# Performance work log

Measured on AMD Instinct MI355X. Metric: run time of the kernel, lower is better.

Reference implementation:

```python
import jax, jax.numpy as jnp
import numpy as np
from jax import lax

# Building physics constants from metadata defaults (sqft=2000)
C_VAL = 300000.0 * 2000.0          # 6e8 J/K
R_VAL = 1.0 / (0.001 * 2000.0)     # 0.5 K/W
T_SET = (70.0 - 32.0) * 5.0 / 9.0  # ~21.111 C (mean of 68F/72F setpoints)
DELTA_T = 2.0
DT = 3600.0
T0 = 22.0
LAM_RC, LAM_COMFORT, LAM_SMOOTH = 1.0, 0.1, 0.01


def setup_inputs() -> dict:
    key = jax.random.key(0)
    k1, k2, k3 = jax.random.split(key, 3)
    B, T = 2048, 8760
    y_hat = jax.random.normal(k1, (B, T), dtype=jnp.float32)
    y_true = jax.random.normal(k2, (B, T), dtype=jnp.float32)
    T_out = jax.random.normal(k3, (B, T), dtype=jnp.float32)
    return {"y_hat": y_hat, "y_true": y_true, "T_out": T_out}


def _infer_temperature(y_hat, T_out):
    # Linear recurrence: T[t+1] = T[t] + dt/C * ((T_out[t]-T[t])/R + 1000*y_hat[t]/C)
    yW = y_hat * 1000.0
    T0v = jnp.full((y_hat.shape[0],), T0, dtype=y_hat.dtype)

    def step(Tc, inp):
        to_t, yw_t = inp
        Tn = Tc + (DT / C_VAL) * ((to_t - Tc) / R_VAL + yw_t / C_VAL)
        return Tn, Tn

    # scan over time; inputs are (T-1, B)
    _, Ts = lax.scan(step, T0v, (T_out[:, :-1].T, yW[:, :-1].T))
    return jnp.concatenate([T0v[:, None], Ts.T], axis=1)  # (B, T)


def reference(y_hat, y_true, T_out):
    # Data-fitting loss (MSE)
    l_data = jnp.mean((y_hat - y_true) ** 2)

    # Infer indoor temperature from RC dynamics
    T_hat = _infer_temperature(y_hat, T_out)

    # RC energy-balance residual loss
    dT = (T_hat[:, 1:] - T_hat[:, :-1]) / DT
    rhs = (T_out[:, :-1] - T_hat[:, :-1]) / R_VAL + (y_hat[:, :-1] * 1000.0) / C_VAL
    l_rc = jnp.mean((dT - rhs) ** 2)

    # Comfort-zone violation loss
    l_comfort = jnp.mean(jax.nn.relu(jnp.abs(T_hat - T_SET) - DELTA_T))

    # Second-order smoothness loss
    d2y = y_hat[:, 2:] - 2.0 * y_hat[:, 1:-1] + y_hat[:, :-2]
    l_smooth = jnp.mean(d2y ** 2)

    return l_data + LAM_RC * l_rc + LAM_COMFORT * l_comfort + LAM_SMOOTH * l_smooth
```

## Files before the change

kernel.cpp:

```cpp
#include <hip/hip_runtime.h>
#include <math.h>

namespace {

constexpr int B_ROWS = 2048;
constexpr int T_LEN  = 8760;
constexpr int NSTEP  = T_LEN - 1;
constexpr int BT     = 256;
constexpr int SEG    = 8;
constexpr int TILE   = BT * SEG;
constexpr int NTILE  = (T_LEN + TILE - 1) / TILE;

constexpr double dpow(double b, int e) { double r = 1.0; for (int i = 0; i < e; ++i) r *= b; return r; }

constexpr double A_D   = 1.0 - 1.2e-5;
constexpr float  AF    = (float)A_D;
constexpr float  A8F   = (float)dpow(A_D, SEG);
constexpr float  QWAVE = (float)dpow(A_D, SEG * 64);

constexpr float DTC    = 6.0e-6f;
constexpr float INV_R  = 2.0f;
constexpr float YC     = (float)(1000.0 / 6.0e8);
constexpr float INV_DT = (float)(1.0 / 3600.0);
constexpr float TSET   = (float)((70.0 - 32.0) * 5.0 / 9.0);
constexpr float TINIT  = 22.0f;

constexpr float W_DATA = (float)(1.0  / ((double)B_ROWS * T_LEN));
constexpr float W_RC   = (float)(1.0  / ((double)B_ROWS * (T_LEN - 1)));
constexpr float W_COMF = (float)(0.1  / ((double)B_ROWS * T_LEN));
constexpr float W_SM   = (float)(0.01 / ((double)B_ROWS * (T_LEN - 2)));

}

__global__ __launch_bounds__(BT) void pinn_main(const float* __restrict__ yh,
                                                const float* __restrict__ ytrue,
                                                const float* __restrict__ tout,
                                                float* __restrict__ ws) {
  const int tid  = threadIdx.x;
  const int lane = tid & 63;
  const int wv   = tid >> 6;
  const size_t rowoff = (size_t)blockIdx.x * T_LEN;
  const float* __restrict__ yr = yh    + rowoff;
  const float* __restrict__ ur = ytrue + rowoff;
  const float* __restrict__ tr = tout  + rowoff;

  float Alane = 1.0f;
  {
    float p = A8F; int e = lane;
    #pragma unroll
    for (int it = 0; it < 6; ++it) { if (e & 1) Alane *= p; p *= p; e >>= 1; }
  }

  __shared__ float sWave[4];
  __shared__ float sRed[4];

  float accData = 0.f, accRc = 0.f, accComf = 0.f, accSm = 0.f;
  float Ttile = TINIT;

  for (int tile = 0; tile < NTILE; ++tile) {
    const int segStart = tile * TILE + tid * SEG;
    const bool inb = segStart < T_LEN;
    float yv[SEG], tv[SEG];

    if (inb) {
      const float4 a0 = *reinterpret_cast<const float4*>(yr + segStart);
      const float4 a1 = *reinterpret_cast<const float4*>(yr + segStart + 4);
      const float4 b0 = *reinterpret_cast<const float4*>(tr + segStart);
      const float4 b1 = *reinterpret_cast<const float4*>(tr + segStart + 4);
      const float4 c0 = *reinterpret_cast<const float4*>(ur + segStart);
      const float4 c1 = *reinterpret_cast<const float4*>(ur + segStart + 4);
      yv[0]=a0.x; yv[1]=a0.y; yv[2]=a0.z; yv[3]=a0.w;
      yv[4]=a1.x; yv[5]=a1.y; yv[6]=a1.z; yv[7]=a1.w;
      tv[0]=b0.x; tv[1]=b0.y; tv[2]=b0.z; tv[3]=b0.w;
      tv[4]=b1.x; tv[5]=b1.y; tv[6]=b1.z; tv[7]=b1.w;
      float uv[SEG];
      uv[0]=c0.x; uv[1]=c0.y; uv[2]=c0.z; uv[3]=c0.w;
      uv[4]=c1.x; uv[5]=c1.y; uv[6]=c1.z; uv[7]=c1.w;
      #pragma unroll
      for (int i = 0; i < SEG; ++i) { const float d = yv[i] - uv[i]; accData += d * d; }
    } else {
      #pragma unroll
      for (int i = 0; i < SEG; ++i) { yv[i] = 0.f; tv[i] = 0.f; }
    }

    float yn0 = 0.f, yn1 = 0.f;
    if (inb && (segStart + SEG) < T_LEN) {
      yn0 = yr[segStart + SEG];
      yn1 = yr[segStart + SEG + 1];
    }

    if (inb) {
      #pragma unroll
      for (int i = 0; i < SEG; ++i) {
        const int t = segStart + i;
        if (t < T_LEN - 2) {
          const float y1 = (i < SEG - 1) ? yv[i + 1] : yn0;
          const float y2 = (i < SEG - 2) ? yv[i + 2] : ((i == SEG - 2) ? yn0 : yn1);
          const float d2 = y2 - 2.f * y1 + yv[i];
          accSm += d2 * d2;
        }
      }
    }

    float S = 0.f;
    #pragma unroll
    for (int i = 0; i < SEG; ++i) {
      const float f = DTC * (tv[i] * INV_R + yv[i] * YC);
      S = AF * S + f;
    }

    float inc = S;
    float m = A8F;
    #pragma unroll
    for (int d = 1; d < 64; d <<= 1) {
      const float up = __shfl_up(inc, (unsigned)d, 64);
      if (lane >= d) inc += m * up;
      m *= m;
    }
    float Eex = __shfl_up(inc, 1u, 64);
    if (lane == 0) Eex = 0.f;

    if (lane == 63) sWave[wv] = inc;
    __syncthreads();

    float W = Ttile;
    for (int v = 0; v < wv; ++v) W = QWAVE * W + sWave[v];
    float Tnext = Ttile;
    #pragma unroll
    for (int v = 0; v < 4; ++v) Tnext = QWAVE * Tnext + sWave[v];
    __syncthreads();
    Ttile = Tnext;

    float Tc = Alane * W + Eex;
    if (inb) {
      #pragma unroll
      for (int i = 0; i < SEG; ++i) {
        const int t = segStart + i;
        if (t < NSTEP) {
          const float rhs = (tv[i] - Tc) * INV_R + yv[i] * YC;
          const float Tnv = Tc + DTC * rhs;
          const float r = (Tnv - Tc) * INV_DT - rhs;
          accRc += r * r;
          const float c = fabsf(Tc - TSET) - 2.0f;
          accComf += (c > 0.f) ? c : 0.f;
          if (t == NSTEP - 1) {
            const float c2 = fabsf(Tnv - TSET) - 2.0f;
            accComf += (c2 > 0.f) ? c2 : 0.f;
          }
          Tc = Tnv;
        }
      }
    }
  }

  float total = accData * W_DATA + accRc * W_RC + accComf * W_COMF + accSm * W_SM;
  #pragma unroll
  for (int d = 32; d > 0; d >>= 1) total += __shfl_down(total, (unsigned)d, 64);
  if (lane == 0) sRed[wv] = total;
  __syncthreads();
  if (tid == 0) ws[blockIdx.x] = sRed[0] + sRed[1] + sRed[2] + sRed[3];
}

__global__ __launch_bounds__(256) void pinn_reduce(const float* __restrict__ ws,
                                                   float* __restrict__ out) {
  const int tid = threadIdx.x;
  float s = 0.f;
  for (int i = tid; i < B_ROWS; i += 256) s += ws[i];
  #pragma unroll
  for (int d = 32; d > 0; d >>= 1) s += __shfl_down(s, (unsigned)d, 64);
  __shared__ float sr[4];
  if ((tid & 63) == 0) sr[tid >> 6] = s;
  __syncthreads();
  if (tid == 0) out[0] = sr[0] + sr[1] + sr[2] + sr[3];
}

extern "C" void kernel_launch(void* const* d_in, const int* in_sizes, int n_in,
                              void* d_out, int out_size, void* d_ws, size_t ws_size,
                              hipStream_t stream) {
  const float* yh    = (const float*)d_in[0];
  const float* ytrue = (const float*)d_in[1];
  const float* tou   = (const float*)d_in[2];
  float* ws = (float*)d_ws;

  pinn_main<<<B_ROWS, BT, 0, stream>>>(yh, ytrue, tou, ws);
  pinn_reduce<<<1, 256, 0, stream>>>(ws, (float*)d_out);
}
```

Baseline: 41.39 us.

## Assign one wavefront per row to drop block barriers and prefetch next tile

Each wavefront now processes a whole row on its own, four rows per block, so the per-tile cross-wave carry through shared memory and both __syncthreads are removed. The carry between tiles is now passed with wave shuffles. The next tile's loads are software-prefetched into registers while the current tile is computed. The extra smoothness-boundary global loads are replaced by lane shuffles plus a carry of the previous tile's last two values. The trade-off is twice the tile count per wave, a longer serial dependency chain per row, and higher register pressure from double-buffered inputs.

```diff
diff --git a/kernel.cpp b/kernel.cpp
--- a/kernel.cpp
+++ b/kernel.cpp
@@ -6,17 +6,18 @@
 constexpr int B_ROWS = 2048;
 constexpr int T_LEN  = 8760;
 constexpr int NSTEP  = T_LEN - 1;
-constexpr int BT     = 256;
 constexpr int SEG    = 8;
-constexpr int TILE   = BT * SEG;
-constexpr int NTILE  = (T_LEN + TILE - 1) / TILE;
+constexpr int TILE   = 64 * SEG;
+constexpr int NT     = (T_LEN + TILE - 1) / TILE;
+constexpr int RPB    = 4;
+constexpr int BT     = 64 * RPB;
 
 constexpr double dpow(double b, int e) { double r = 1.0; for (int i = 0; i < e; ++i) r *= b; return r; }
 
 constexpr double A_D   = 1.0 - 1.2e-5;
 constexpr float  AF    = (float)A_D;
 constexpr float  A8F   = (float)dpow(A_D, SEG);
-constexpr float  QWAVE = (float)dpow(A_D, SEG * 64);
+constexpr float  QTILE = (float)dpow(A_D, TILE);
 
 constexpr float DTC    = 6.0e-6f;
 constexpr float INV_R  = 2.0f;
@@ -39,7 +40,8 @@
   const int tid  = threadIdx.x;
   const int lane = tid & 63;
   const int wv   = tid >> 6;
-  const size_t rowoff = (size_t)blockIdx.x * T_LEN;
+  const int row  = blockIdx.x * RPB + wv;
+  const size_t rowoff = (size_t)row * T_LEN;
   const float* __restrict__ yr = yh    + rowoff;
   const float* __restrict__ ur = ytrue + rowoff;
   const float* __restrict__ tr = tout  + rowoff;
@@ -51,49 +53,78 @@
     for (int it = 0; it < 6; ++it) { if (e & 1) Alane *= p; p *= p; e >>= 1; }
   }
 
-  __shared__ float sWave[4];
-  __shared__ float sRed[4];
-
   float accData = 0.f, accRc = 0.f, accComf = 0.f, accSm = 0.f;
-  float Ttile = TINIT;
-
-  for (int tile = 0; tile < NTILE; ++tile) {
-    const int segStart = tile * TILE + tid * SEG;
-    const bool inb = segStart < T_LEN;
-    float yv[SEG], tv[SEG];
-
-    if (inb) {
-      const float4 a0 = *reinterpret_cast<const float4*>(yr + segStart);
-      const float4 a1 = *reinterpret_cast<const float4*>(yr + segStart + 4);
-      const float4 b0 = *reinterpret_cast<const float4*>(tr + segStart);
-      const float4 b1 = *reinterpret_cast<const float4*>(tr + segStart + 4);
-      const float4 c0 = *reinterpret_cast<const float4*>(ur + segStart);
-      const float4 c1 = *reinterpret_cast<const float4*>(ur + segStart + 4);
-      yv[0]=a0.x; yv[1]=a0.y; yv[2]=a0.z; yv[3]=a0.w;
-      yv[4]=a1.x; yv[5]=a1.y; yv[6]=a1.z; yv[7]=a1.w;
-      tv[0]=b0.x; tv[1]=b0.y; tv[2]=b0.z; tv[3]=b0.w;
-      tv[4]=b1.x; tv[5]=b1.y; tv[6]=b1.z; tv[7]=b1.w;
-      float uv[SEG];
-      uv[0]=c0.x; uv[1]=c0.y; uv[2]=c0.z; uv[3]=c0.w;
-      uv[4]=c1.x; uv[5]=c1.y; uv[6]=c1.z; uv[7]=c1.w;
+  float Tstart = TINIT;
+  float ypv0 = 0.f, ypv1 = 0.f;
+
+  float ny[SEG], ntv[SEG], nu[SEG];
+
+  {
+    const int ss = lane * SEG;
+    const float4 a0 = *reinterpret_cast<const float4*>(yr + ss);
+    const float4 a1 = *reinterpret_cast<const float4*>(yr + ss + 4);
+    const float4 b0 = *reinterpret_cast<const float4*>(tr + ss);
+    const float4 b1 = *reinterpret_cast<const float4*>(tr + ss + 4);
+    const float4 c0 = *reinterpret_cast<const float4*>(ur + ss);
+    const float4 c1 = *reinterpret_cast<const float4*>(ur + ss + 4);
+    ny[0]=a0.x; ny[1]=a0.y; ny[2]=a0.z; ny[3]=a0.w;
+    ny[4]=a1.x; ny[5]=a1.y; ny[6]=a1.z; ny[7]=a1.w;
+    ntv[0]=b0.x; ntv[1]=b0.y; ntv[2]=b0.z; ntv[3]=b0.w;
+    ntv[4]=b1.x; ntv[5]=b1.y; ntv[6]=b1.z; ntv[7]=b1.w;
+    nu[0]=c0.x; nu[1]=c0.y; nu[2]=c0.z; nu[3]=c0.w;
+    nu[4]=c1.x; nu[5]=c1.y; nu[6]=c1.z; nu[7]=c1.w;
+  }
+
+  for (int t = 0; t < NT; ++t) {
+    float yv[SEG], tv[SEG], uv[SEG];
+    #pragma unroll
+    for (int i = 0; i < SEG; ++i) { yv[i] = ny[i]; tv[i] = ntv[i]; uv[i] = nu[i]; }
+
+    if (t + 1 < NT) {
+      const int ss = (t + 1) * TILE + lane * SEG;
+      const bool inb = ss < T_LEN;
+      if (inb) {
+        const float4 a0 = *reinterpret_cast<const float4*>(yr + ss);
+        const float4 a1 = *reinterpret_cast<const float4*>(yr + ss + 4);
+        const float4 b0 = *reinterpret_cast<const float4*>(tr + ss);
+        const float4 b1 = *reinterpret_cast<const float4*>(tr + ss + 4);
+        const float4 c0 = *reinterpret_cast<const float4*>(ur + ss);
+        const float4 c1 = *reinterpret_cast<const float4*>(ur + ss + 4);
+        ny[0]=a0.x; ny[1]=a0.y; ny[2]=a0.z; ny[3]=a0.w;
+        ny[4]=a1.x; ny[5]=a1.y; ny[6]=a1.z; ny[7]=a1.w;
+        ntv[0]=b0.x; ntv[1]=b0.y; ntv[2]=b0.z; ntv[3]=b0.w;
+        ntv[4]=b1.x; ntv[5]=b1.y; ntv[6]=b1.z; ntv[7]=b1.w;
+        nu[0]=c0.x; nu[1]=c0.y; nu[2]=c0.z; nu[3]=c0.w;
+        nu[4]=c1.x; nu[5]=c1.y; nu[6]=c1.z; nu[7]=c1.w;
+      } else {
+        #pragma unroll
+        for (int i = 0; i < SEG; ++i) { ny[i] = 0.f; ntv[i] = 0.f; nu[i] = 0.f; }
+      }
+    }
+
+    const int segStart = t * TILE + lane * SEG;
+    const bool act = segStart < T_LEN;
+
+    if (act) {
       #pragma unroll
       for (int i = 0; i < SEG; ++i) { const float d = yv[i] - uv[i]; accData += d * d; }
-    } else {
-      #pragma unroll
-      for (int i = 0; i < SEG; ++i) { yv[i] = 0.f; tv[i] = 0.f; }
-    }
-
-    float yn0 = 0.f, yn1 = 0.f;
-    if (inb && (segStart + SEG) < T_LEN) {
-      yn0 = yr[segStart + SEG];
-      yn1 = yr[segStart + SEG + 1];
-    }
-
-    if (inb) {
+    }
+
+    const float yn0 = __shfl_down(yv[0], 1u, 64);
+    const float yn1 = __shfl_down(yv[1], 1u, 64);
+
+    if (t > 0 && lane == 0) {
+      const float d2a = yv[0] - 2.f * ypv1 + ypv0;
+      const float d2b = yv[1] - 2.f * yv[0] + ypv1;
+      accSm += d2a * d2a + d2b * d2b;
+    }
+
+    if (act) {
       #pragma unroll
       for (int i = 0; i < SEG; ++i) {
-        const int t = segStart + i;
-        if (t < T_LEN - 2) {
+        const int tt = segStart + i;
+        const bool needN = (i >= SEG - 2);
+        if (tt < T_LEN - 2 && (!needN || lane < 63)) {
           const float y1 = (i < SEG - 1) ? yv[i + 1] : yn0;
           const float y2 = (i < SEG - 2) ? yv[i + 2] : ((i == SEG - 2) ? yn0 : yn1);
           const float d2 = y2 - 2.f * y1 + yv[i];
@@ -119,31 +150,24 @@
     }
     float Eex = __shfl_up(inc, 1u, 64);
     if (lane == 0) Eex = 0.f;
-
-    if (lane == 63) sWave[wv] = inc;
-    __syncthreads();
-
-    float W = Ttile;
-    for (int v = 0; v < wv; ++v) W = QWAVE * W + sWave[v];
-    float Tnext = Ttile;
-    #pragma unroll
-    for (int v = 0; v < 4; ++v) Tnext = QWAVE * Tnext + sWave[v];
-    __syncthreads();
-    Ttile = Tnext;
-
-    float Tc = Alane * W + Eex;
-    if (inb) {
+    const float Stot = __shfl(inc, 63, 64);
+
+    ypv0 = __shfl(yv[6], 63, 64);
+    ypv1 = __shfl(yv[7], 63, 64);
+
+    float Tc = Alane * Tstart + Eex;
+    if (act) {
       #pragma unroll
       for (int i = 0; i < SEG; ++i) {
-        const int t = segStart + i;
-        if (t < NSTEP) {
+        const int tt = segStart + i;
+        if (tt < NSTEP) {
           const float rhs = (tv[i] - Tc) * INV_R + yv[i] * YC;
           const float Tnv = Tc + DTC * rhs;
           const float r = (Tnv - Tc) * INV_DT - rhs;
           accRc += r * r;
           const float c = fabsf(Tc - TSET) - 2.0f;
           accComf += (c > 0.f) ? c : 0.f;
-          if (t == NSTEP - 1) {
+          if (tt == NSTEP - 1) {
             const float c2 = fabsf(Tnv - TSET) - 2.0f;
             accComf += (c2 > 0.f) ? c2 : 0.f;
           }
@@ -151,14 +175,14 @@
         }
       }
     }
+
+    Tstart = QTILE * Tstart + Stot;
   }
 
   float total = accData * W_DATA + accRc * W_RC + accComf * W_COMF + accSm * W_SM;
   #pragma unroll
   for (int d = 32; d > 0; d >>= 1) total += __shfl_down(total, (unsigned)d, 64);
-  if (lane == 0) sRed[wv] = total;
-  __syncthreads();
-  if (tid == 0) ws[blockIdx.x] = sRed[0] + sRed[1] + sRed[2] + sRed[3];
+  if (lane == 0) ws[row] = total;
 }
 
 __global__ __launch_bounds__(256) void pinn_reduce(const float* __restrict__ ws,
@@ -182,6 +206,6 @@
   const float* tou   = (const float*)d_in[2];
   float* ws = (float*)d_ws;
 
-  pinn_main<<<B_ROWS, BT, 0, stream>>>(yh, ytrue, tou, ws);
+  pinn_main<<<B_ROWS / RPB, BT, 0, stream>>>(yh, ytrue, tou, ws);
   pinn_reduce<<<1, 256, 0, stream>>>(ws, (float*)d_out);
 }
```

Measured after the change: 41.01 us. About the same (-0.9%).
